# Kernel tuning notes

Hardware: AMD Instinct MI355X
Metric: run time of the kernel (lower is better)

The kernel has to match this reference:

```python
import jax, jax.numpy as jnp
import numpy as np


def _morpho(x, weight, bias, sign, padding, stride):
    # x: [B,C,H,W], weight: [B,C,kh,kw], bias: [B,C], sign: [B]
    B, C, H, W = x.shape
    kh, kw = weight.shape[-2:]
    # sign handling: if |sign| >= 1e-7 multiply by sign, else leave unchanged
    m = (jnp.abs(sign) >= 1e-7).astype(x.dtype)          # [B], constant (detached in torch)
    s = m * sign + (1.0 - m)                              # effective multiplier per sample
    xs = x * s[:, None, None, None]
    # unfold zero-pads, and sign*0 == 0, so padding signed x with zeros is equivalent
    xp = jnp.pad(xs, ((0, 0), (0, 0), (padding, padding), (padding, padding)))
    H2 = (H + 2 * padding - kh) // stride + 1
    W2 = (W + 2 * padding - kw) // stride + 1
    # direct windowed max-plus: y[b,c,i,j] = max_{p,q} xs_pad[b,c,i*s+p,j*s+q] + w[b,c,p,q]
    # small fixed kh*kw loop avoids materializing the B*C*kh*kw*L unfold tensor
    y = jnp.full((B, C, H2, W2), -jnp.inf, dtype=x.dtype)
    for p in range(kh):
        for q in range(kw):
            patch = jax.lax.slice(
                xp,
                (0, 0, p, q),
                (B, C, p + (H2 - 1) * stride + 1, q + (W2 - 1) * stride + 1),
                (1, 1, stride, stride),
            )  # [B,C,H2,W2]
            y = jnp.maximum(y, patch + weight[:, :, p, q][:, :, None, None])
    y = y + bias[:, :, None, None]
    return y * s[:, None, None, None]


def setup_inputs() -> dict:
    key = jax.random.key(0)
    k1, k2, k3, k4 = jax.random.split(key, 4)
    B, C, H, W, kh, kw = 16, 64, 128, 128, 5, 5
    return {
        "x": jax.random.normal(k1, (B, C, H, W), dtype=jnp.float32),
        "weight": jax.random.normal(k2, (B, C, kh, kw), dtype=jnp.float32) * 0.1,
        "bias": jax.random.normal(k3, (B, C), dtype=jnp.float32) * 0.1,
        "sign": jax.random.normal(k4, (B,), dtype=jnp.float32),
        "padding": 2,
        "stride": 1,
    }


def reference(x, weight, bias, sign, padding, stride):
    return _morpho(x, weight, bias, sign, padding, stride)
```

## Files before the change

### kernel.cpp

```cpp
#include <hip/hip_runtime.h>
#include <math.h>

#define HB 16
#define CB 64
#define HH 128
#define WW 128
#define NFLOATS (HB * CB * HH * WW)

__global__ __launch_bounds__(256) void morpho_kernel(
    const float* __restrict__ x,
    const float* __restrict__ w,
    const float* __restrict__ bias,
    const float* __restrict__ sign,
    float* __restrict__ out)
{
    const int blk  = blockIdx.x;
    const int quad = blk & 3;
    const int bc   = blk >> 2;
    const int b    = bc >> 6;

    float*       __restrict__ yp = out + (size_t)bc * (HH * WW);
    const float* __restrict__ wp = w   + bc * 25;

    const float sgn = sign[b];
    const float s   = (fabsf(sgn) >= 1e-7f) ? sgn : 1.0f;
    const float bv  = bias[bc];

    float wv[25];
#pragma unroll
    for (int k = 0; k < 25; ++k) wv[k] = wp[k];

    const int t  = threadIdx.x;
    const int tx = t & 31;
    const int ty = t >> 5;
    const int j0 = tx * 4;
    const int i0 = quad * 32 + ty * 4;

    const float sL = (tx >= 1)  ? s : 0.f;
    const float sR = (tx <= 30) ? s : 0.f;

    const int planeOff = bc * (HH * WW);

    float acc[4][4];

#pragma unroll
    for (int r8 = 0; r8 < 8; ++r8) {
        const int r  = i0 - 2 + r8;
        const bool rv = ((unsigned)r < (unsigned)HH);
        const float smM = rv ? s  : 0.f;
        const float smL = rv ? sL : 0.f;
        const float smR = rv ? sR : 0.f;

        int oM = planeOff + r * WW + j0;
        int oL = oM - 4;
        int oR = oM + 4;
        oL = min(max(oL, 0), NFLOATS - 4);
        oM = min(max(oM, 0), NFLOATS - 4);
        oR = min(max(oR, 0), NFLOATS - 4);

        const float4 v0 = *reinterpret_cast<const float4*>(x + oL);
        const float4 v1 = *reinterpret_cast<const float4*>(x + oM);
        const float4 v2 = *reinterpret_cast<const float4*>(x + oR);

        float xr[12];
        xr[0]  = v0.x * smL; xr[1]  = v0.y * smL; xr[2]  = v0.z * smL; xr[3]  = v0.w * smL;
        xr[4]  = v1.x * smM; xr[5]  = v1.y * smM; xr[6]  = v1.z * smM; xr[7]  = v1.w * smM;
        xr[8]  = v2.x * smR; xr[9]  = v2.y * smR; xr[10] = v2.z * smR; xr[11] = v2.w * smR;

#pragma unroll
        for (int p = 0; p < 5; ++p) {
            const int oi = r8 - p;
            if (oi >= 0 && oi < 4) {
#pragma unroll
                for (int oj = 0; oj < 4; ++oj) {
                    const float t0 = xr[oj + 2] + wv[p * 5 + 0];
                    const float t1 = xr[oj + 3] + wv[p * 5 + 1];
                    const float t2 = xr[oj + 4] + wv[p * 5 + 2];
                    const float t3 = xr[oj + 5] + wv[p * 5 + 3];
                    const float t4 = xr[oj + 6] + wv[p * 5 + 4];
                    float m;
                    if (p == 0) {
                        m = fmaxf(fmaxf(t0, t1), t2);
                        m = fmaxf(fmaxf(m, t3), t4);
                    } else {
                        m = acc[oi][oj];
                        m = fmaxf(fmaxf(m, t0), t1);
                        m = fmaxf(fmaxf(m, t2), t3);
                        m = fmaxf(m, t4);
                    }
                    acc[oi][oj] = m;
                }
            }
        }
    }

#pragma unroll
    for (int a = 0; a < 4; ++a) {
        float4 o;
        o.x = (acc[a][0] + bv) * s;
        o.y = (acc[a][1] + bv) * s;
        o.z = (acc[a][2] + bv) * s;
        o.w = (acc[a][3] + bv) * s;
        *reinterpret_cast<float4*>(yp + (size_t)(i0 + a) * WW + j0) = o;
    }
}

extern "C" void kernel_launch(void* const* d_in, const int* in_sizes, int n_in,
                              void* d_out, int out_size, void* d_ws, size_t ws_size,
                              hipStream_t stream) {
    const float* x    = (const float*)d_in[0];
    const float* w    = (const float*)d_in[1];
    const float* bias = (const float*)d_in[2];
    const float* sign = (const float*)d_in[3];
    float* out = (float*)d_out;

    const int planes = HB * CB;
    const int grid   = planes * 4;
    morpho_kernel<<<grid, 256, 0, stream>>>(x, w, bias, sign, out);
}
```

Measured before the change: 32.17 us.

## Stage padded, sign-scaled input tile in LDS before windowed max-plus

```diff
diff --git a/kernel.cpp b/kernel.cpp
--- a/kernel.cpp
+++ b/kernel.cpp
@@ -5,7 +5,11 @@
 #define CB 64
 #define HH 128
 #define WW 128
-#define NFLOATS (HB * CB * HH * WW)
+
+#define LROWS 36
+#define LCOLS 136
+#define LELEM (LROWS * LCOLS)
+#define LQUADS (LROWS * (LCOLS / 4))
 
 __global__ __launch_bounds__(256) void morpho_kernel(
     const float* __restrict__ x,
@@ -14,11 +18,14 @@
     const float* __restrict__ sign,
     float* __restrict__ out)
 {
+    __shared__ float lds[LELEM];
+
     const int blk  = blockIdx.x;
     const int quad = blk & 3;
     const int bc   = blk >> 2;
     const int b    = bc >> 6;
 
+    const float* __restrict__ xp = x   + (size_t)bc * (HH * WW);
     float*       __restrict__ yp = out + (size_t)bc * (HH * WW);
     const float* __restrict__ wp = w   + bc * 25;
 
@@ -26,46 +33,52 @@
     const float s   = (fabsf(sgn) >= 1e-7f) ? sgn : 1.0f;
     const float bv  = bias[bc];
 
+    const int t       = threadIdx.x;
+    const int rowbase = quad * 32 - 2;
+
+#pragma unroll
+    for (int k = 0; k < 5; ++k) {
+        const int i = k * 256 + t;
+        if (i < LQUADS) {
+            const int r    = i / 34;
+            const int c4   = i - r * 34;
+            const int grow = rowbase + r;
+            const int gcol = c4 * 4 - 4;
+            const bool valid = ((unsigned)grow < (unsigned)HH) &&
+                               ((unsigned)(c4 - 1) < 32u);
+            const float sm = valid ? s : 0.f;
+            const int rc = min(max(grow, 0), HH - 1);
+            const int cc = min(max(gcol, 0), WW - 4);
+            const float4 v = *reinterpret_cast<const float4*>(xp + rc * WW + cc);
+            float4 o;
+            o.x = v.x * sm; o.y = v.y * sm; o.z = v.z * sm; o.w = v.w * sm;
+            *reinterpret_cast<float4*>(&lds[r * LCOLS + c4 * 4]) = o;
+        }
+    }
+
     float wv[25];
 #pragma unroll
     for (int k = 0; k < 25; ++k) wv[k] = wp[k];
 
-    const int t  = threadIdx.x;
+    __syncthreads();
+
     const int tx = t & 31;
     const int ty = t >> 5;
     const int j0 = tx * 4;
     const int i0 = quad * 32 + ty * 4;
 
-    const float sL = (tx >= 1)  ? s : 0.f;
-    const float sR = (tx <= 30) ? s : 0.f;
-
-    const int planeOff = bc * (HH * WW);
-
     float acc[4][4];
 
 #pragma unroll
     for (int r8 = 0; r8 < 8; ++r8) {
-        const int r  = i0 - 2 + r8;
-        const bool rv = ((unsigned)r < (unsigned)HH);
-        const float smM = rv ? s  : 0.f;
-        const float smL = rv ? sL : 0.f;
-        const float smR = rv ? sR : 0.f;
-
-        int oM = planeOff + r * WW + j0;
-        int oL = oM - 4;
-        int oR = oM + 4;
-        oL = min(max(oL, 0), NFLOATS - 4);
-        oM = min(max(oM, 0), NFLOATS - 4);
-        oR = min(max(oR, 0), NFLOATS - 4);
-
-        const float4 v0 = *reinterpret_cast<const float4*>(x + oL);
-        const float4 v1 = *reinterpret_cast<const float4*>(x + oM);
-        const float4 v2 = *reinterpret_cast<const float4*>(x + oR);
-
+        const float* lp = &lds[(ty * 4 + r8) * LCOLS + tx * 4];
+        const float4 a0 = *reinterpret_cast<const float4*>(lp);
+        const float4 a1 = *reinterpret_cast<const float4*>(lp + 4);
+        const float4 a2 = *reinterpret_cast<const float4*>(lp + 8);
         float xr[12];
-        xr[0]  = v0.x * smL; xr[1]  = v0.y * smL; xr[2]  = v0.z * smL; xr[3]  = v0.w * smL;
-        xr[4]  = v1.x * smM; xr[5]  = v1.y * smM; xr[6]  = v1.z * smM; xr[7]  = v1.w * smM;
-        xr[8]  = v2.x * smR; xr[9]  = v2.y * smR; xr[10] = v2.z * smR; xr[11] = v2.w * smR;
+        xr[0] = a0.x; xr[1] = a0.y; xr[2]  = a0.z; xr[3]  = a0.w;
+        xr[4] = a1.x; xr[5] = a1.y; xr[6]  = a1.z; xr[7]  = a1.w;
+        xr[8] = a2.x; xr[9] = a2.y; xr[10] = a2.z; xr[11] = a2.w;
 
 #pragma unroll
         for (int p = 0; p < 5; ++p) {
```

Result: slower. 35.34 us (+9.9%).
